# Kernel tuning notes

Hardware: AMD Instinct MI355X
Metric: run time of the kernel (lower is better)

Reference implementation:

```python
import jax, jax.numpy as jnp
import numpy as np

H = 128  # hidden size
F_IN = 33  # GRU input size
STEPS = 64


def setup_inputs() -> dict:
    key = jax.random.key(0)
    ks = jax.random.split(key, 10)
    x = jax.random.normal(ks[0], (STEPS, 17), dtype=jnp.float32)
    ip = jax.random.randint(ks[1], (STEPS, 8), 0, 256)
    port = jax.random.randint(ks[2], (STEPS, 2), 0, 70000)
    hidden = jnp.zeros((1, 1, H), dtype=jnp.float32)
    # learned parameters (torch default init ~ U(-1/sqrt(H), 1/sqrt(H)) for GRU, N(0,1) for embeddings)
    s = 1.0 / np.sqrt(H)
    ip_emb = jax.random.normal(ks[3], (256, 1), dtype=jnp.float32)
    port_emb = jax.random.normal(ks[4], (70000, 4), dtype=jnp.float32)
    W_ih = jax.random.uniform(ks[5], (3 * H, F_IN), minval=-s, maxval=s, dtype=jnp.float32)
    W_hh = jax.random.uniform(ks[6], (3 * H, H), minval=-s, maxval=s, dtype=jnp.float32)
    b_ih = jax.random.uniform(ks[7], (3 * H,), minval=-s, maxval=s, dtype=jnp.float32)
    b_hh = jax.random.uniform(ks[8], (3 * H,), minval=-s, maxval=s, dtype=jnp.float32)
    return {"x": x, "ip": ip, "port": port, "hidden": hidden,
            "ip_emb": ip_emb, "port_emb": port_emb,
            "W_ih": W_ih, "W_hh": W_hh, "b_ih": b_ih, "b_hh": b_hh}


def reference(x, ip, port, hidden, ip_emb, port_emb, W_ih, W_hh, b_ih, b_hh):
    # Embedding lookups + flatten: [64, 8*1] and [64, 2*4]
    ipf = ip_emb[ip].reshape(STEPS, -1)
    pf = port_emb[port].reshape(STEPS, -1)
    xi = jnp.concatenate([x, ipf, pf], axis=1)  # [64, 33]
    h0 = hidden[0, 0]  # [128]; same initial hidden reused at every step in the original loop
    # Single batched GRU cell over all 64 "steps" (they are independent given shared h0)
    gi = xi @ W_ih.T + b_ih          # [64, 3H]
    gh = h0 @ W_hh.T + b_hh          # [3H], broadcast over the 64 rows
    i_r, i_z, i_n = jnp.split(gi, 3, axis=1)
    h_r, h_z, h_n = jnp.split(gh, 3)
    r = jax.nn.sigmoid(i_r + h_r)
    z = jax.nn.sigmoid(i_z + h_z)
    n = jnp.tanh(i_n + r * h_n)
    outputs = (1.0 - z) * n + z * h0  # [64, 128]
    new_hidden = outputs[STEPS - 1].reshape(1, 1, H)  # self.hidden after last iteration
    return outputs, new_hidden
```

## Files before the change

kernel.cpp:

```cpp
#include <hip/hip_runtime.h>
#include <hip/hip_bf16.h>

#define H 128
#define STEPS 64
#define F_IN 33

__global__ __launch_bounds__(H) void Encoder_57380763074770_kernel(
    const float* __restrict__ x,
    const int*   __restrict__ ip,
    const int*   __restrict__ port,
    const float* __restrict__ hidden,
    const float* __restrict__ ip_emb,
    const float* __restrict__ port_emb,
    const float* __restrict__ W_ih,
    const float* __restrict__ W_hh,
    const float* __restrict__ b_ih,
    const float* __restrict__ b_hh,
    float* __restrict__ out)
{
    __shared__ float xi[F_IN];
    __shared__ float h0[H];

    const int s = blockIdx.x;
    const int j = threadIdx.x;

    if (j < 17) {
        xi[j] = x[s * 17 + j];
    } else if (j < 25) {
        xi[j] = ip_emb[ip[s * 8 + (j - 17)]];
    } else if (j < F_IN) {
        int c = j - 25;
        xi[j] = port_emb[port[s * 2 + (c >> 2)] * 4 + (c & 3)];
    }
    h0[j] = hidden[j];
    __syncthreads();

    float ghr = b_hh[j];
    float ghz = b_hh[j + H];
    float ghn = b_hh[j + 2 * H];
    const float* wr = W_hh + (size_t)j * H;
    const float* wz = W_hh + (size_t)(j + H) * H;
    const float* wn = W_hh + (size_t)(j + 2 * H) * H;
    #pragma unroll 8
    for (int k = 0; k < H; ++k) {
        float h = h0[k];
        ghr = fmaf(h, wr[k], ghr);
        ghz = fmaf(h, wz[k], ghz);
        ghn = fmaf(h, wn[k], ghn);
    }

    float gir = b_ih[j];
    float giz = b_ih[j + H];
    float gin = b_ih[j + 2 * H];
    const float* vr = W_ih + (size_t)j * F_IN;
    const float* vz = W_ih + (size_t)(j + H) * F_IN;
    const float* vn = W_ih + (size_t)(j + 2 * H) * F_IN;
    #pragma unroll
    for (int k = 0; k < F_IN; ++k) {
        float xv = xi[k];
        gir = fmaf(xv, vr[k], gir);
        giz = fmaf(xv, vz[k], giz);
        gin = fmaf(xv, vn[k], gin);
    }

    float r = 1.0f / (1.0f + expf(-(gir + ghr)));
    float z = 1.0f / (1.0f + expf(-(giz + ghz)));
    float n = tanhf(gin + r * ghn);
    float o = (1.0f - z) * n + z * h0[j];

    out[s * H + j] = o;
    if (s == STEPS - 1) out[STEPS * H + j] = o;
}

extern "C" void kernel_launch(void* const* d_in, const int* in_sizes, int n_in,
                              void* d_out, int out_size, void* d_ws, size_t ws_size,
                              hipStream_t stream) {
    const float* x        = (const float*)d_in[0];
    const int*   ip       = (const int*)  d_in[1];
    const int*   port     = (const int*)  d_in[2];
    const float* hidden   = (const float*)d_in[3];
    const float* ip_emb   = (const float*)d_in[4];
    const float* port_emb = (const float*)d_in[5];
    const float* W_ih     = (const float*)d_in[6];
    const float* W_hh     = (const float*)d_in[7];
    const float* b_ih     = (const float*)d_in[8];
    const float* b_hh     = (const float*)d_in[9];
    float* out = (float*)d_out;

    Encoder_57380763074770_kernel<<<STEPS, H, 0, stream>>>(
        x, ip, port, hidden, ip_emb, port_emb, W_ih, W_hh, b_ih, b_hh, out);
}
```

Baseline: 80.06 us.

## Coalesce W_hh matvec with wave reductions and stage W_ih in shared memory

Rewrites the hidden-state matvec so each wave reads W_hh rows with contiguous lanes and reduces the partial sums via shuffle, instead of each thread striding through its own row. W_ih is copied into shared memory with float4 loads so the input projection no longer does strided global reads. Also swaps expf/tanhf for fast __expf-based formulas with a clamp. The cost is serialized shuffle reductions over 192 rows per wave, a large LDS footprint (~50KB), and slightly lower activation precision.

```diff
diff --git a/kernel.cpp b/kernel.cpp
--- a/kernel.cpp
+++ b/kernel.cpp
@@ -4,8 +4,9 @@
 #define H 128
 #define STEPS 64
 #define F_IN 33
+#define R3H 384
 
-__global__ __launch_bounds__(H) void Encoder_57380763074770_kernel(
+__global__ __launch_bounds__(128) void Encoder_57380763074770_kernel(
     const float* __restrict__ x,
     const int*   __restrict__ ip,
     const int*   __restrict__ port,
@@ -19,54 +20,74 @@
     float* __restrict__ out)
 {
     __shared__ float xi[F_IN];
-    __shared__ float h0[H];
+    __shared__ float h0s[H];
+    __shared__ float ghs[R3H];
+    __shared__ float wih[R3H * F_IN];
 
-    const int s = blockIdx.x;
-    const int j = threadIdx.x;
+    const int s    = blockIdx.x;
+    const int tid  = threadIdx.x;
+    const int lane = tid & 63;
+    const int wave = tid >> 6;
 
-    if (j < 17) {
-        xi[j] = x[s * 17 + j];
-    } else if (j < 25) {
-        xi[j] = ip_emb[ip[s * 8 + (j - 17)]];
-    } else if (j < F_IN) {
-        int c = j - 25;
-        xi[j] = port_emb[port[s * 2 + (c >> 2)] * 4 + (c & 3)];
+    if (tid < 17) {
+        xi[tid] = x[s * 17 + tid];
+    } else if (tid < 25) {
+        xi[tid] = ip_emb[ip[s * 8 + (tid - 17)]];
+    } else if (tid < F_IN) {
+        int c = tid - 25;
+        xi[tid] = port_emb[port[s * 2 + (c >> 2)] * 4 + (c & 3)];
     }
-    h0[j] = hidden[j];
+    h0s[tid] = hidden[tid];
+
+    {
+        const float4* w4 = (const float4*)W_ih;
+        float4*       l4 = (float4*)wih;
+        for (int i = tid; i < (R3H * F_IN) / 4; i += 128) l4[i] = w4[i];
+    }
     __syncthreads();
 
-    float ghr = b_hh[j];
-    float ghz = b_hh[j + H];
-    float ghn = b_hh[j + 2 * H];
-    const float* wr = W_hh + (size_t)j * H;
-    const float* wz = W_hh + (size_t)(j + H) * H;
-    const float* wn = W_hh + (size_t)(j + 2 * H) * H;
-    #pragma unroll 8
-    for (int k = 0; k < H; ++k) {
-        float h = h0[k];
-        ghr = fmaf(h, wr[k], ghr);
-        ghz = fmaf(h, wz[k], ghz);
-        ghn = fmaf(h, wn[k], ghn);
+    {
+        const float h0a = h0s[lane];
+        const float h0b = h0s[lane + 64];
+        const int base = wave * 192;
+        #pragma unroll 4
+        for (int i = 0; i < 192; ++i) {
+            const int row = base + i;
+            const float* wrow = W_hh + (size_t)row * H;
+            float p = fmaf(h0a, wrow[lane], h0b * wrow[lane + 64]);
+            #pragma unroll
+            for (int m = 32; m >= 1; m >>= 1) p += __shfl_xor(p, m, 64);
+            if (lane == 0) ghs[row] = p;
+        }
     }
+    __syncthreads();
 
+    const int j = tid;
     float gir = b_ih[j];
     float giz = b_ih[j + H];
     float gin = b_ih[j + 2 * H];
-    const float* vr = W_ih + (size_t)j * F_IN;
-    const float* vz = W_ih + (size_t)(j + H) * F_IN;
-    const float* vn = W_ih + (size_t)(j + 2 * H) * F_IN;
+    const float* vr = wih + j * F_IN;
+    const float* vz = wih + (j + H) * F_IN;
+    const float* vn = wih + (j + 2 * H) * F_IN;
     #pragma unroll
     for (int k = 0; k < F_IN; ++k) {
-        float xv = xi[k];
+        const float xv = xi[k];
         gir = fmaf(xv, vr[k], gir);
         giz = fmaf(xv, vz[k], giz);
         gin = fmaf(xv, vn[k], gin);
     }
 
-    float r = 1.0f / (1.0f + expf(-(gir + ghr)));
-    float z = 1.0f / (1.0f + expf(-(giz + ghz)));
-    float n = tanhf(gin + r * ghn);
-    float o = (1.0f - z) * n + z * h0[j];
+    const float ghr = ghs[j]         + b_hh[j];
+    const float ghz = ghs[j + H]     + b_hh[j + H];
+    const float ghn = ghs[j + 2 * H] + b_hh[j + 2 * H];
+
+    const float r = 1.0f / (1.0f + __expf(-(gir + ghr)));
+    const float z = 1.0f / (1.0f + __expf(-(giz + ghz)));
+    float a = gin + r * ghn;
+    a = fminf(fmaxf(a, -15.0f), 15.0f);
+    const float e2 = __expf(2.0f * a);
+    const float n = (e2 - 1.0f) / (e2 + 1.0f);
+    const float o = (1.0f - z) * n + z * h0s[j];
 
     out[s * H + j] = o;
     if (s == STEPS - 1) out[STEPS * H + j] = o;
```

Result: slower. 160.0 us (+99.8%).
